# Optimization experiments

Measured on AMD Instinct MI355X. Metric: run time of the kernel, lower is better.

## Reference

```python
import jax, jax.numpy as jnp
import numpy as np

BETA = 0.01
EPS = 1e-6

def conv3x3(x, w, b):
    y = jax.lax.conv_general_dilated(x, w, (1, 1), 'SAME',
                                     dimension_numbers=('NCHW', 'OIHW', 'NCHW'))
    return y + b[None, :, None, None]

def variance_depth_flow(gt, patch, max_depth):
    B, C, H, W = gt.shape
    py, px = H // patch, W // patch
    # [B,C,py,px,P,P]
    p = gt.reshape(B, C, py, patch, px, patch).transpose(0, 1, 2, 4, 3, 5)
    p = jnp.where((p > 0.1) & (p < max_depth), p, jnp.zeros_like(p))
    bn = jnp.log(p[..., 0, :] + EPS)   # north border  [B,C,py,px,P]
    bs = jnp.log(p[..., -1, :] + EPS)  # south
    bw = jnp.log(p[..., :, 0] + EPS)   # west
    be = jnp.log(p[..., :, -1] + EPS)  # east
    def sx(b):  # shift patches left along x (axis=3), zero-pad last column
        return jnp.concatenate([b[:, :, :, 1:], jnp.zeros_like(b[:, :, :, :1])], axis=3)
    def sy(b):  # shift patches up along y (axis=2), zero-pad last row
        return jnp.concatenate([b[:, :, 1:], jnp.zeros_like(b[:, :, :1])], axis=2)
    diffs = [be - sx(bw), bs - sy(bn), be - sx(be), bs - sy(bs), bw - sx(bw),
             bn - sy(bn), bs - sx(bs), be - sy(be), bn - sx(bn), bw - sy(bw)]
    d = jnp.stack([x.sum(-1) for x in diffs], axis=-1)  # [B,C,py,px,10]
    d = d[:, 0].transpose(0, 3, 1, 2) / patch            # [B,10,py,px]
    return d

def smooth_l1(pred, target, beta):
    d = pred - target
    ad = jnp.abs(d)
    return jnp.where(ad < beta, 0.5 * d * d / beta, ad - 0.5 * beta)

def setup_inputs() -> dict:
    key = jax.random.key(0)
    ks = jax.random.split(key, 7)
    B, FC, DC, hw, HW = 32, 256, 64, 64, 512
    feat = jax.random.normal(ks[0], (B, FC, hw, hw), dtype=jnp.float32)
    depth = jax.random.normal(ks[1], (B, DC, hw, hw), dtype=jnp.float32)
    gts = jax.random.uniform(ks[2], (B, 1, HW, HW), dtype=jnp.float32)
    W_att = jax.random.normal(ks[3], (DC, FC, 3, 3), dtype=jnp.float32) * 0.02
    b_att = jnp.zeros((DC,), dtype=jnp.float32)
    W_post = jax.random.normal(ks[4], (10, DC, 3, 3), dtype=jnp.float32) * 0.05
    b_post = jnp.zeros((10,), dtype=jnp.float32)
    return {"feat": feat, "depth": depth, "gts": gts,
            "W_att": W_att, "b_att": b_att, "W_post": W_post, "b_post": b_post}

def reference(feat, depth, gts, W_att, b_att, W_post, b_post):
    max_depth = 80.0
    n, c, h, w = depth.shape
    patch = gts.shape[2] // h
    flow_gradient = variance_depth_flow(gts, patch, max_depth)  # [B,10,h,w]
    att = jax.nn.sigmoid(conv3x3(feat, W_att, b_att))           # [B,DC,h,w]
    ds = conv3x3(att * depth, W_post, b_post)                   # [B,10,h,w]
    diff = smooth_l1(ds, flow_gradient, BETA)
    return diff.sum() / (h * w * ds.shape[0] * ds.shape[1])
```

## Files before the change

### kernel.cpp

```cpp
#include <hip/hip_runtime.h>
#include <hip/hip_bf16.h>


typedef __attribute__((ext_vector_type(4))) float f32x4;
typedef __attribute__((ext_vector_type(8))) short s16x8;
typedef __attribute__((ext_vector_type(4))) unsigned int u32x4;

#define DEVFN __device__ __forceinline__

DEVFN float bf2f(unsigned short u){
  unsigned int x = ((unsigned int)u) << 16;
  float f; __builtin_memcpy(&f, &x, 4); return f;
}
DEVFN unsigned short f2bf(float f){
  unsigned int x; __builtin_memcpy(&x, &f, 4);
  x += 0x7fffu + ((x >> 16) & 1u);
  return (unsigned short)(x >> 16);
}
DEVFN unsigned cvtpk(float lo, float hi){
  unsigned r;
  asm("v_cvt_pk_bf16_f32 %0, %1, %2" : "=v"(r) : "v"(lo), "v"(hi));
  return r;
}

#define ASYNC16(gp, lp) __builtin_amdgcn_global_load_lds( \
    (const __attribute__((address_space(1))) unsigned int*)(gp), \
    (__attribute__((address_space(3))) unsigned int*)(lp), 16, 0, 0)

__global__ void k_weights(const float* __restrict__ Watt, const float* __restrict__ Wpost,
                          unsigned short* __restrict__ WT1, unsigned short* __restrict__ WT2){
  const int t = blockIdx.x * 256 + threadIdx.x;
  const int n1 = 9 * 64 * 256;
  if (t < n1){
    const int tap = t / (64 * 256);
    const int rem = t % (64 * 256);
    const int oc = rem / 256, ic = rem % 256;
    WT1[t] = f2bf(Watt[(oc * 256 + ic) * 9 + tap]);
  }
  const int n2 = 9 * 16 * 64;
  if (t < n2){
    const int tap = t / (16 * 64);
    const int rem = t % (16 * 64);
    const int od = rem / 64, ic = rem % 64;
    const float v = (od < 10) ? Wpost[(od * 64 + ic) * 9 + tap] : 0.0f;
    WT2[t] = f2bf(v);
  }
}

__global__ void k_borders(const float* __restrict__ gts, float* __restrict__ S,
                          float* __restrict__ out){
  const int bid = blockIdx.x, tid = threadIdx.x;
  if (bid == 0 && tid == 0) *out = 0.0f;
  __shared__ float slab[4096];
  const int rel = bid;
  const float* gp = gts + (size_t)rel * 4096;
#pragma unroll
  for (int it = 0; it < 4; ++it){
    const int id = it * 256 + tid;
    *(f32x4*)&slab[id * 4] = *(const f32x4*)&gp[id * 4];
  }
  __syncthreads();
  const int px = tid & 63, border = tid >> 6;
  float s = 0.0f;
#pragma unroll
  for (int i = 0; i < 8; ++i){
    float v;
    if (border == 0)      v = slab[px * 8 + i];
    else if (border == 1) v = slab[7 * 512 + px * 8 + i];
    else if (border == 2) v = slab[i * 512 + px * 8];
    else                  v = slab[i * 512 + px * 8 + 7];
    v = ((v > 0.1f) && (v < 80.0f)) ? v : 0.0f;
    s += __logf(v + 1e-6f);
  }
  S[((size_t)rel * 64 + px) * 4 + border] = s;
}

__global__ __launch_bounds__(256, 2) void k_gemm1(
    const float* __restrict__ feat,
    const unsigned short* __restrict__ WT1,
    const float* __restrict__ batt,
    const float* __restrict__ depth,
    unsigned short* __restrict__ adT)
{
  __shared__ unsigned short As[6 * 66 * 40];
  __shared__ unsigned short Bs[576 * 32];
  const int t = threadIdx.x;
  const int l = t & 63, w = t >> 6;
  const int b = blockIdx.x >> 4, ytile = blockIdx.x & 15;
  const int y0 = ytile * 4;
  const int fr = l & 15, g = l >> 4;

  f32x4 acc[4][4];
#pragma unroll
  for (int i = 0; i < 4; ++i)
#pragma unroll
    for (int j = 0; j < 4; ++j)
#pragma unroll
      for (int q = 0; q < 4; ++q) acc[i][j][q] = 0.0f;

  if (t < 48){
    const int yy = t >> 3, k = t & 7;
    const int xp = (k & 1) ? 65 : 0;
    u32x4 z = {0, 0, 0, 0};
    *(u32x4*)&As[(yy * 66 + xp) * 40 + ((k >> 1) & 3) * 8] = z;
  }

  auto loadRow = [&](int c, int yy, f32x4* v){
    const int yr = y0 - 1 + yy;
    if (yr >= 0 && yr < 64){
      const float* gp = feat + ((size_t)(b * 256 + c * 32 + g * 8)) * 4096
                             + (size_t)yr * 64 + fr * 4;
#pragma unroll
      for (int e = 0; e < 8; ++e) v[e] = *(const f32x4*)(gp + (size_t)e * 4096);
    } else {
#pragma unroll
      for (int e = 0; e < 8; ++e) v[e] = f32x4{0.f, 0.f, 0.f, 0.f};
    }
  };
  auto cvtWriteRow = [&](int yy, const f32x4* v){
#pragma unroll
    for (int o = 0; o < 4; ++o){
      const int xp = fr * 4 + o + 1;
      u32x4 pk;
      pk[0] = cvtpk(v[0][o], v[1][o]);
      pk[1] = cvtpk(v[2][o], v[3][o]);
      pk[2] = cvtpk(v[4][o], v[5][o]);
      pk[3] = cvtpk(v[6][o], v[7][o]);
      *(u32x4*)&As[(yy * 66 + xp) * 40 + g * 8] = pk;
    }
  };
  auto stageB = [&](int c){
#pragma unroll
    for (int it = 0; it < 9; ++it){
      const int idx = it * 256 + t;
      const int row = idx >> 2;
      const int sg = (idx & 3) ^ ((row >> 1) & 3);
      ASYNC16(WT1 + (size_t)row * 256 + c * 32 + sg * 8, &Bs[(size_t)idx * 8]);
    }
  };
  auto compute = [&](){
    const int slotB = (g ^ ((fr >> 1) & 3)) * 8;
#pragma unroll
    for (int tap = 0; tap < 9; ++tap){
      const int dy = tap / 3 - 1, dxp = tap % 3;
      const int yy = w + dy + 1;
      s16x8 af[4], bfr[4];
#pragma unroll
      for (int i = 0; i < 4; ++i)
        af[i] = *(const s16x8*)&As[(yy * 66 + (i * 16 + fr + dxp)) * 40 + g * 8];
#pragma unroll
      for (int j = 0; j < 4; ++j)
        bfr[j] = *(const s16x8*)&Bs[(tap * 64 + j * 16 + fr) * 32 + slotB];
#pragma unroll
      for (int i = 0; i < 4; ++i)
#pragma unroll
        for (int j = 0; j < 4; ++j)
          acc[i][j] = __builtin_amdgcn_mfma_f32_16x16x32_bf16(af[i], bfr[j], acc[i][j], 0, 0, 0);
    }
  };

  f32x4 r0[8], r1[8];
  loadRow(0, w, r0);
  if (w < 2) loadRow(0, 4 + w, r1);
  stageB(0);
  cvtWriteRow(w, r0);
  if (w < 2) cvtWriteRow(4 + w, r1);
  __syncthreads();

  for (int c = 0; c < 8; ++c){
    if (c < 7){
      loadRow(c + 1, w, r0);
      if (w < 2) loadRow(c + 1, 4 + w, r1);
    }
    compute();
    __syncthreads();
    if (c < 7){
      cvtWriteRow(w, r0);
      if (w < 2) cvtWriteRow(4 + w, r1);
      stageB(c + 1);
    }
    __syncthreads();
  }

  const int y = y0 + w;
#pragma unroll
  for (int j = 0; j < 4; ++j){
    const int oc = j * 16 + fr;
    const float bb = batt[oc];
    const float* dpt = depth + ((size_t)(b * 64 + oc)) * 4096 + (size_t)y * 64;
    unsigned short* op = adT + ((size_t)(b * 4096 + y * 64)) * 64 + oc;
#pragma unroll
    for (int i = 0; i < 4; ++i){
      const f32x4 dv4 = *(const f32x4*)&dpt[i * 16 + g * 4];
#pragma unroll
      for (int q = 0; q < 4; ++q){
        const int xo = i * 16 + g * 4 + q;
        const float v = acc[i][j][q] + bb;
        const float att = 1.0f / (1.0f + __expf(-v));
        op[(size_t)xo * 64] = f2bf(att * dv4[q]);
      }
    }
  }
}

DEVFN float sel4(f32x4 v, int i){
  const float ab = (i & 1) ? v[1] : v[0];
  const float cd = (i & 1) ? v[3] : v[2];
  return (i & 2) ? cd : ab;
}

__global__ __launch_bounds__(512, 2) void k_gemm2(
    const unsigned short* __restrict__ adT,
    const unsigned short* __restrict__ WT2,
    const float* __restrict__ bpost,
    const f32x4* __restrict__ S,
    float* __restrict__ out)
{
  __shared__ unsigned short As[2][20480];
  __shared__ unsigned short Bs[9216];
  __shared__ float ps[8];
  const int t = threadIdx.x;
  const int l = t & 63, w = t >> 6;
  const int b = blockIdx.x >> 3, ytile = blockIdx.x & 7;
  const int y0 = ytile * 8;
  const int fr = l & 15, g = l >> 4;

  f32x4 acc[4];
#pragma unroll
  for (int i = 0; i < 4; ++i)
#pragma unroll
    for (int q = 0; q < 4; ++q) acc[i][q] = 0.0f;

  auto stageA = [&](int c, int d){
#pragma unroll
    for (int it2 = 0; it2 < 5; ++it2){
      const int it = it2 * 2 + (t >> 8);
      const int yy = y0 - 1 + it;
      const int xx = (t >> 2) & 63, icg = t & 3;
      unsigned short* lp = &As[d][(it * 64 + xx) * 32 + icg * 8];
      if (yy >= 0 && yy < 64){
        const int sg = icg ^ ((xx >> 1) & 3);
        const unsigned short* gp = adT
            + ((size_t)(b * 4096 + yy * 64 + xx)) * 64 + c * 32 + sg * 8;
        ASYNC16(gp, lp);
      } else {
        s16x8 z = {0,0,0,0,0,0,0,0};
        *(s16x8*)lp = z;
      }
    }
  };
#pragma unroll
  for (int it = 0; it < 3; ++it){
    const int idx = it * 512 + t;
    if (idx < 1152){
      const int row = idx >> 3, p = idx & 7;
      const int sg = p ^ (row & 7);
      ASYNC16(WT2 + (size_t)row * 64 + sg * 8, Bs + (size_t)idx * 8);
    }
  }
  stageA(0, 0);
  __syncthreads();

  for (int c = 0; c < 2; ++c){
    if (c == 0) stageA(1, 1);
    const unsigned short* Ab = As[c];
    const int pB = ((c * 4 + g) ^ (fr & 7)) * 8;
    for (int tap = 0; tap < 9; ++tap){
      const int dy = tap / 3 - 1, dx = tap % 3 - 1;
      s16x8 af[4];
#pragma unroll
      for (int i = 0; i < 4; ++i){
        const int xv = i * 16 + fr + dx;
        const bool valid = (xv >= 0) && (xv < 64);
        const int xw = valid ? xv : 0;
        const int slot = (g ^ ((xw >> 1) & 3)) * 8;
        s16x8 v = *(const s16x8*)&Ab[((w + dy + 1) * 64 + xw) * 32 + slot];
        s16x8 z = {0,0,0,0,0,0,0,0};
        af[i] = valid ? v : z;
      }
      const s16x8 bfr = *(const s16x8*)&Bs[(tap * 16 + fr) * 64 + pB];
#pragma unroll
      for (int i = 0; i < 4; ++i)
        acc[i] = __builtin_amdgcn_mfma_f32_16x16x32_bf16(af[i], bfr, acc[i], 0, 0, 0);
    }
    __syncthreads();
  }

  const unsigned aPack = (3u<<0)|(1u<<2)|(3u<<4)|(1u<<6)|(2u<<8)|(0u<<10)|(1u<<12)|(3u<<14)|(0u<<16)|(2u<<18);
  const unsigned bPack = (2u<<0)|(0u<<2)|(3u<<4)|(1u<<6)|(2u<<8)|(0u<<10)|(1u<<12)|(3u<<14)|(0u<<16)|(2u<<18);
  float lsum = 0.0f;
  const int y = y0 + w;
  if (fr < 10){
    const int od = fr;
    const int ai = (aPack >> (2 * od)) & 3;
    const int bi = (bPack >> (2 * od)) & 3;
    const bool xshift = (od & 1) == 0;
    const float bp = bpost[od];
#pragma unroll
    for (int i = 0; i < 4; ++i){
#pragma unroll
      for (int q = 0; q < 4; ++q){
        const int xo = i * 16 + g * 4 + q;
        const size_t gm = (size_t)b * 4096 + (size_t)y * 64 + xo;
        const f32x4 sa = S[gm];
        const bool nb = xshift ? (xo < 63) : (y < 63);
        const size_t ga = xshift ? (nb ? gm + 1 : gm) : (nb ? gm + 64 : gm);
        const f32x4 sbv = S[ga];
        const float sbf = nb ? sel4(sbv, bi) : 0.0f;
        const float flow = (sel4(sa, ai) - sbf) * 0.125f;
        const float dv = acc[i][q] + bp - flow;
        const float adv = fabsf(dv);
        lsum += (adv < 0.01f) ? (50.0f * dv * dv) : (adv - 0.005f);
      }
    }
  }
#pragma unroll
  for (int off = 32; off > 0; off >>= 1) lsum += __shfl_down(lsum, off);
  if (l == 0) ps[w] = lsum;
  __syncthreads();
  if (t == 0){
    float s = 0.0f;
#pragma unroll
    for (int i = 0; i < 8; ++i) s += ps[i];
    atomicAdd(out, s * (1.0f / 1310720.0f));
  }
}

extern "C" void kernel_launch(void* const* d_in, const int* in_sizes, int n_in,
                              void* d_out, int out_size, void* d_ws, size_t ws_size,
                              hipStream_t stream){
  const float* feat  = (const float*)d_in[0];
  const float* depth = (const float*)d_in[1];
  const float* gts   = (const float*)d_in[2];
  const float* Watt  = (const float*)d_in[3];
  const float* batt  = (const float*)d_in[4];
  const float* Wpost = (const float*)d_in[5];
  const float* bpost = (const float*)d_in[6];
  float* out = (float*)d_out;
  char* ws = (char*)d_ws;

  unsigned short* adT = (unsigned short*)ws;
  unsigned short* WT1 = (unsigned short*)(ws + 16777216);
  unsigned short* WT2 = (unsigned short*)(ws + 16777216 + 294912);
  float*          S   = (float*)(ws + 16777216 + 294912 + 18432);

  k_weights<<<576, 256, 0, stream>>>(Watt, Wpost, WT1, WT2);
  k_gemm1<<<512, 256, 0, stream>>>(feat, WT1, batt, depth, adT);
  k_borders<<<2048, 256, 0, stream>>>(gts, S, out);
  k_gemm2<<<256, 512, 0, stream>>>(adT, WT2, bpost, (const f32x4*)S, out);
}
```

Measured before the change: 87.98 us.

## Double-buffer per-tap weight tiles and pipeline A loads across taps in conv GEMM

Result: slower. 105.3 us (+19.7%).

```diff
diff --git a/kernel.cpp b/kernel.cpp
--- a/kernel.cpp
+++ b/kernel.cpp
@@ -7,6 +7,11 @@
 typedef __attribute__((ext_vector_type(4))) unsigned int u32x4;
 
 #define DEVFN __device__ __forceinline__
+
+#define VMW(N) asm volatile("s_waitcnt vmcnt(" #N ")" ::: "memory")
+#define LGKM0() asm volatile("s_waitcnt lgkmcnt(0)" ::: "memory")
+#define BAR() __builtin_amdgcn_s_barrier()
+#define SCHEDB() __builtin_amdgcn_sched_barrier(0)
 
 DEVFN float bf2f(unsigned short u){
   unsigned int x = ((unsigned int)u) << 16;
@@ -83,7 +88,7 @@
     unsigned short* __restrict__ adT)
 {
   __shared__ unsigned short As[6 * 66 * 40];
-  __shared__ unsigned short Bs[576 * 32];
+  __shared__ unsigned short Bs[2][64 * 32];
   const int t = threadIdx.x;
   const int l = t & 63, w = t >> 6;
   const int b = blockIdx.x >> 4, ytile = blockIdx.x & 15;
@@ -105,81 +110,87 @@
     *(u32x4*)&As[(yy * 66 + xp) * 40 + ((k >> 1) & 3) * 8] = z;
   }
 
-  auto loadRow = [&](int c, int yy, f32x4* v){
-    const int yr = y0 - 1 + yy;
-    if (yr >= 0 && yr < 64){
-      const float* gp = feat + ((size_t)(b * 256 + c * 32 + g * 8)) * 4096
-                             + (size_t)yr * 64 + fr * 4;
-#pragma unroll
-      for (int e = 0; e < 8; ++e) v[e] = *(const f32x4*)(gp + (size_t)e * 4096);
-    } else {
-#pragma unroll
-      for (int e = 0; e < 8; ++e) v[e] = f32x4{0.f, 0.f, 0.f, 0.f};
-    }
-  };
-  auto cvtWriteRow = [&](int yy, const f32x4* v){
-#pragma unroll
-    for (int o = 0; o < 4; ++o){
-      const int xp = fr * 4 + o + 1;
-      u32x4 pk;
-      pk[0] = cvtpk(v[0][o], v[1][o]);
-      pk[1] = cvtpk(v[2][o], v[3][o]);
-      pk[2] = cvtpk(v[4][o], v[5][o]);
-      pk[3] = cvtpk(v[6][o], v[7][o]);
-      *(u32x4*)&As[(yy * 66 + xp) * 40 + g * 8] = pk;
-    }
-  };
-  auto stageB = [&](int c){
-#pragma unroll
-    for (int it = 0; it < 9; ++it){
-      const int idx = it * 256 + t;
-      const int row = idx >> 2;
-      const int sg = (idx & 3) ^ ((row >> 1) & 3);
-      ASYNC16(WT1 + (size_t)row * 256 + c * 32 + sg * 8, &Bs[(size_t)idx * 8]);
-    }
-  };
-  auto compute = [&](){
+  f32x4 hold[3][4];
+  auto loadA = [&](int c){
+#pragma unroll
+    for (int uu = 0; uu < 3; ++uu){
+      const int u = w * 3 + uu, row = u >> 1, eh = u & 1;
+      const int yr = y0 - 1 + row;
+      if (yr >= 0 && yr < 64){
+        const float* gp = feat + ((size_t)(b * 256 + c * 32 + g * 8 + eh * 4)) * 4096
+                               + (size_t)yr * 64 + fr * 4;
+#pragma unroll
+        for (int k = 0; k < 4; ++k) hold[uu][k] = *(const f32x4*)(gp + (size_t)k * 4096);
+      } else {
+#pragma unroll
+        for (int k = 0; k < 4; ++k) hold[uu][k] = f32x4{0.f, 0.f, 0.f, 0.f};
+      }
+    }
+  };
+  auto cvtWriteA = [&](){
+#pragma unroll
+    for (int uu = 0; uu < 3; ++uu){
+      const int u = w * 3 + uu, row = u >> 1, eh = u & 1;
+#pragma unroll
+      for (int o = 0; o < 4; ++o){
+        const int xp = fr * 4 + o + 1;
+        const unsigned lo = cvtpk(hold[uu][0][o], hold[uu][1][o]);
+        const unsigned hi = cvtpk(hold[uu][2][o], hold[uu][3][o]);
+        const unsigned long long v = ((unsigned long long)hi << 32) | lo;
+        *(unsigned long long*)&As[(row * 66 + xp) * 40 + g * 8 + eh * 4] = v;
+      }
+    }
+  };
+  auto stageBtap = [&](int p){
+    const int cc = p / 9, tp = p - cc * 9;
+    const int row = t >> 2, sl = t & 3;
+    const int sg = sl ^ ((row >> 1) & 3);
+    ASYNC16(WT1 + (size_t)(tp * 64 + row) * 256 + cc * 32 + sg * 8,
+            &Bs[p & 1][(size_t)t * 8]);
+  };
+  auto compute = [&](int tap, int buf){
+    const int dy = tap / 3 - 1, dxp = tap % 3;
+    const int yy = w + dy + 1;
     const int slotB = (g ^ ((fr >> 1) & 3)) * 8;
+    s16x8 af[4], bfr[4];
+#pragma unroll
+    for (int i = 0; i < 4; ++i)
+      af[i] = *(const s16x8*)&As[(yy * 66 + (i * 16 + fr + dxp)) * 40 + g * 8];
+#pragma unroll
+    for (int j = 0; j < 4; ++j)
+      bfr[j] = *(const s16x8*)&Bs[buf][(j * 16 + fr) * 32 + slotB];
+#pragma unroll
+    for (int i = 0; i < 4; ++i)
+#pragma unroll
+      for (int j = 0; j < 4; ++j)
+        acc[i][j] = __builtin_amdgcn_mfma_f32_16x16x32_bf16(af[i], bfr[j], acc[i][j], 0, 0, 0);
+  };
+
+  loadA(0);
+  stageBtap(0);
+  VMW(1);
+  cvtWriteA();
+  LGKM0();
+
+  for (int c = 0; c < 8; ++c){
 #pragma unroll
     for (int tap = 0; tap < 9; ++tap){
-      const int dy = tap / 3 - 1, dxp = tap % 3;
-      const int yy = w + dy + 1;
-      s16x8 af[4], bfr[4];
-#pragma unroll
-      for (int i = 0; i < 4; ++i)
-        af[i] = *(const s16x8*)&As[(yy * 66 + (i * 16 + fr + dxp)) * 40 + g * 8];
-#pragma unroll
-      for (int j = 0; j < 4; ++j)
-        bfr[j] = *(const s16x8*)&Bs[(tap * 64 + j * 16 + fr) * 32 + slotB];
-#pragma unroll
-      for (int i = 0; i < 4; ++i)
-#pragma unroll
-        for (int j = 0; j < 4; ++j)
-          acc[i][j] = __builtin_amdgcn_mfma_f32_16x16x32_bf16(af[i], bfr[j], acc[i][j], 0, 0, 0);
-    }
-  };
-
-  f32x4 r0[8], r1[8];
-  loadRow(0, w, r0);
-  if (w < 2) loadRow(0, 4 + w, r1);
-  stageB(0);
-  cvtWriteRow(w, r0);
-  if (w < 2) cvtWriteRow(4 + w, r1);
-  __syncthreads();
-
-  for (int c = 0; c < 8; ++c){
+      const int p = c * 9 + tap;
+      if (tap == 0 && c < 7) loadA(c + 1);
+      if (p < 71) stageBtap(p + 1);
+      if (c < 7)        VMW(13);
+      else if (tap < 8) VMW(1);
+      else              VMW(0);
+      BAR();
+      SCHEDB();
+      compute(tap, p & 1);
+    }
+    BAR();
     if (c < 7){
-      loadRow(c + 1, w, r0);
-      if (w < 2) loadRow(c + 1, 4 + w, r1);
-    }
-    compute();
-    __syncthreads();
-    if (c < 7){
-      cvtWriteRow(w, r0);
-      if (w < 2) cvtWriteRow(4 + w, r1);
-      stageB(c + 1);
-    }
-    __syncthreads();
+      VMW(1);
+      cvtWriteA();
+      LGKM0();
+    }
   }
 
   const int y = y0 + w;
```
